# Kernel tuning notes

Hardware: AMD Instinct MI355X
Metric: run time of the kernel (lower is better)

## Reference

```python
import jax, jax.numpy as jnp
import numpy as np
from jax import lax

D_MODEL = 1024
D_STATE = 16
D_CONV = 4
D_INNER = 2 * D_MODEL
BATCH = 2
SEQ = 1024


def setup_inputs() -> dict:
    key = jax.random.key(0)
    ks = jax.random.split(key, 8)
    std = 0.02
    return {
        "x": jax.random.normal(ks[0], (BATCH, SEQ, D_MODEL), jnp.float32),
        "in_proj_w": jax.random.normal(ks[1], (2 * D_INNER, D_MODEL), jnp.float32) * std,
        "conv_w": jax.random.normal(ks[2], (D_INNER, 1, D_CONV), jnp.float32) * 0.1,
        "x_proj_w": jax.random.normal(ks[3], (D_STATE + 1, D_INNER), jnp.float32) * std,
        "dt_w": jax.random.normal(ks[4], (D_INNER, 1), jnp.float32) * std,
        "dt_b": jnp.zeros((D_INNER,), jnp.float32),
        "A_param": jax.random.normal(ks[5], (D_INNER, D_STATE), jnp.float32) * std,
        "D_param": jnp.ones((D_INNER,), jnp.float32),
        "out_w": jax.random.normal(ks[6], (D_MODEL, D_INNER), jnp.float32) * std,
        "out_b": jnp.zeros((D_MODEL,), jnp.float32),
    }


def _silu(v):
    return v * jax.nn.sigmoid(v)


def _mamba_forward(x, in_proj_w, conv_w, x_proj_w, dt_w, dt_b, A_param, D_param, out_w, out_b):
    B, L, _ = x.shape
    # in_proj: [B,L,2*d_inner]
    xz = jnp.einsum('bld,ed->ble', x, in_proj_w)
    u, z = jnp.split(xz, 2, axis=-1)  # each [B,L,d_inner]
    # depthwise causal conv1d along time
    uc = u.transpose(0, 2, 1)  # [B,d_inner,L]
    uc = lax.conv_general_dilated(
        uc, conv_w, window_strides=(1,), padding=[(D_CONV - 1, D_CONV - 1)],
        dimension_numbers=('NCH', 'OIH', 'NCH'), feature_group_count=D_INNER,
    )[:, :, :L]
    u = _silu(uc.transpose(0, 2, 1))  # [B,L,d_inner]
    # x_proj -> (dt scalar, B coeffs)
    x_dbl = jnp.einsum('bld,ed->ble', u, x_proj_w)  # [B,L,d_state+1]
    dt_in = x_dbl[..., :1]                          # [B,L,1]
    Bmat = x_dbl[..., 1:]                           # [B,L,d_state]
    delta = jax.nn.softplus(dt_in * dt_w[:, 0] + dt_b)  # [B,L,d_inner]
    A = -jnp.exp(A_param)                            # [d_inner,d_state]

    # selective scan (time-major lax.scan)
    def step(h, inp):
        d_t, b_t = inp  # [B,d_inner], [B,d_state]
        h = jnp.exp(A * d_t[..., None]) * h + d_t[..., None] * b_t[:, None, :]
        y = jnp.einsum('bdn,bn->bd', h, b_t)
        return h, y

    h0 = jnp.zeros((B, D_INNER, D_STATE), x.dtype)
    _, ys = lax.scan(step, h0, (delta.transpose(1, 0, 2), Bmat.transpose(1, 0, 2)))
    y = ys.transpose(1, 0, 2) + u * D_param  # [B,L,d_inner]
    y = y * _silu(z)
    return jnp.einsum('bld,ed->ble', y, out_w) + out_b


def reference(x, in_proj_w, conv_w, x_proj_w, dt_w, dt_b, A_param, D_param, out_w, out_b):
    return _mamba_forward(x, in_proj_w, conv_w, x_proj_w, dt_w, dt_b, A_param, D_param, out_w, out_b)
```

## Files before the change

kernel.cpp:

```cpp
#include <hip/hip_runtime.h>
#include <stdint.h>
#include <stddef.h>

#define D_MODEL 1024
#define D_STATE 16
#define D_INNER 2048
#define BATCH   2
#define SEQ     1024
#define MROWS   (BATCH*SEQ)

#define NCH 32
#define TCH (SEQ/NCH)
#define NREC (BATCH*D_INNER*D_STATE)

#define XKS 8
#define XKC (D_INNER/XKS)

typedef __bf16 bf16x8 __attribute__((ext_vector_type(8)));
typedef float  f32x4  __attribute__((ext_vector_type(4)));

__device__ __forceinline__ unsigned short f2bf(float f) {
    unsigned int u = __float_as_uint(f);
    u += 0x7fffu + ((u >> 16) & 1u);
    return (unsigned short)(u >> 16);
}
__device__ __forceinline__ float bf2f(unsigned short v) {
    return __uint_as_float((unsigned int)v << 16);
}

__device__ __forceinline__ void gl_lds16(const unsigned short* g, unsigned short* l) {
    __builtin_amdgcn_global_load_lds(
        (const __attribute__((address_space(1))) unsigned int*)g,
        (__attribute__((address_space(3))) unsigned int*)l, 16, 0, 0);
}

__global__ void cvt_all_kernel(const float* __restrict__ x,
                               const float* __restrict__ w1,
                               const float* __restrict__ w2,
                               const float* __restrict__ xw,
                               unsigned short* __restrict__ xb,
                               unsigned short* __restrict__ wbi,
                               unsigned short* __restrict__ wbo,
                               unsigned short* __restrict__ wbp) {
    int blk = blockIdx.x, tid = threadIdx.x;
    if (blk < 8192) {
        const float* src; unsigned short* dst; int i;
        if (blk < 2048)      { src = x;  dst = xb;  i = blk * 1024 + tid * 4; }
        else if (blk < 6144) { src = w1; dst = wbi; i = (blk - 2048) * 1024 + tid * 4; }
        else                 { src = w2; dst = wbo; i = (blk - 6144) * 1024 + tid * 4; }
        float4 v = *(const float4*)(src + i);
        ushort4 o;
        o.x = f2bf(v.x); o.y = f2bf(v.y); o.z = f2bf(v.z); o.w = f2bf(v.w);
        *(ushort4*)(dst + i) = o;
    } else {
        int id = (blk - 8192) * 256 + tid;
        wbp[id] = (id < 17 * D_INNER) ? f2bf(xw[id]) : (unsigned short)0;
    }
}

template<int NT, bool BIAS>
__global__ void gemm_bf16_kernel(const unsigned short* __restrict__ A,
                                 const unsigned short* __restrict__ Bw,
                                 float* __restrict__ C,
                                 const float* __restrict__ bias,
                                 int M, int N, int K) {
    constexpr int NTW  = NT / 32;
    constexpr int BCHW = NT / 64;
    __shared__ __align__(16) unsigned short Al[128 * 32];
    __shared__ __align__(16) unsigned short Bl[NT * 32];

    const int tid  = threadIdx.x;
    const int lane = tid & 63;
    const int wid  = tid >> 6;
    const int wm   = wid >> 1;
    const int wn   = wid & 1;
    const int ln   = lane & 15;
    const int q    = lane >> 4;
    const int mblk = blockIdx.y * 128;
    const int nblk = blockIdx.x * NT;
    const int srow = lane >> 2;
    const int spart = lane & 3;

    f32x4 acc[4][NTW] = {};

    for (int k0 = 0; k0 < K; k0 += 32) {
        #pragma unroll
        for (int h = 0; h < 2; ++h) {
            int j = wid * 2 + h;
            int row = j * 16 + srow;
            gl_lds16(A + (size_t)(mblk + row) * K + k0 + spart * 8, Al + j * 512);
        }
        #pragma unroll
        for (int h = 0; h < BCHW; ++h) {
            int j = wid * BCHW + h;
            int row = j * 16 + srow;
            gl_lds16(Bw + (size_t)(nblk + row) * K + k0 + spart * 8, Bl + j * 512);
        }
        __syncthreads();

        bf16x8 af[4], bfr[NTW];
        #pragma unroll
        for (int mt = 0; mt < 4; ++mt)
            af[mt] = *(const bf16x8*)(Al + (wm * 64 + mt * 16 + ln) * 32 + q * 8);
        #pragma unroll
        for (int nt = 0; nt < NTW; ++nt)
            bfr[nt] = *(const bf16x8*)(Bl + (wn * (NT/2) + nt * 16 + ln) * 32 + q * 8);

        #pragma unroll
        for (int mt = 0; mt < 4; ++mt)
            #pragma unroll
            for (int nt = 0; nt < NTW; ++nt)
                acc[mt][nt] = __builtin_amdgcn_mfma_f32_16x16x32_bf16(
                    af[mt], bfr[nt], acc[mt][nt], 0, 0, 0);
        __syncthreads();
    }

    #pragma unroll
    for (int mt = 0; mt < 4; ++mt) {
        #pragma unroll
        for (int nt = 0; nt < NTW; ++nt) {
            int col = nblk + wn * (NT/2) + nt * 16 + ln;
            float bv = BIAS ? bias[col] : 0.f;
            #pragma unroll
            for (int r = 0; r < 4; ++r) {
                int row = mblk + wm * 64 + mt * 16 + q * 4 + r;
                C[(size_t)row * N + col] = acc[mt][nt][r] + bv;
            }
        }
    }
}

__global__ void conv_silu_kernel(const float* __restrict__ xz,
                                 const float* __restrict__ conv_w,
                                 unsigned short* __restrict__ ub) {
    int idx = blockIdx.x * blockDim.x + threadIdx.x;
    int d = idx & (D_INNER - 1);
    int m = idx >> 11;
    int l = m & (SEQ - 1);
    const float* w = conv_w + d * 4;
    float s = 0.f;
    #pragma unroll
    for (int j = 0; j < 4; ++j) {
        if (l - j >= 0) s += w[3 - j] * xz[(size_t)(m - j) * 4096 + d];
    }
    float sig = 1.f / (1.f + __expf(-s));
    ub[idx] = f2bf(s * sig);
}

__global__ void xproj_mfma_kernel(const unsigned short* __restrict__ ub,
                                  const unsigned short* __restrict__ wbp,
                                  float* __restrict__ part) {
    __shared__ __align__(16) unsigned short Al[64 * 64];
    __shared__ __align__(16) unsigned short Bl[32 * 64];

    const int tid  = threadIdx.x;
    const int lane = tid & 63;
    const int wid  = tid >> 6;
    const int ln   = lane & 15;
    const int q    = lane >> 4;
    const int m0   = blockIdx.y * 64;
    const int ks   = blockIdx.x;
    const int srow = lane >> 3;
    const int spart = lane & 7;

    f32x4 acc[2] = {};

    for (int it = 0; it < 4; ++it) {
        int k0 = ks * XKC + it * 64;
        #pragma unroll
        for (int h = 0; h < 2; ++h) {
            int j = wid * 2 + h;
            int row = j * 8 + srow;
            gl_lds16(ub + (size_t)(m0 + row) * D_INNER + k0 + spart * 8, Al + j * 512);
        }
        {
            int row = wid * 8 + srow;
            gl_lds16(wbp + (size_t)row * D_INNER + k0 + spart * 8, Bl + wid * 512);
        }
        __syncthreads();

        bf16x8 af[2], bfr[2][2];
        #pragma unroll
        for (int kh = 0; kh < 2; ++kh) {
            af[kh] = *(const bf16x8*)(Al + (wid * 16 + ln) * 64 + kh * 32 + q * 8);
            bfr[0][kh] = *(const bf16x8*)(Bl + (0 * 16 + ln) * 64 + kh * 32 + q * 8);
            bfr[1][kh] = *(const bf16x8*)(Bl + (1 * 16 + ln) * 64 + kh * 32 + q * 8);
        }
        #pragma unroll
        for (int kh = 0; kh < 2; ++kh) {
            acc[0] = __builtin_amdgcn_mfma_f32_16x16x32_bf16(af[kh], bfr[0][kh], acc[0], 0, 0, 0);
            acc[1] = __builtin_amdgcn_mfma_f32_16x16x32_bf16(af[kh], bfr[1][kh], acc[1], 0, 0, 0);
        }
        __syncthreads();
    }

    #pragma unroll
    for (int nf = 0; nf < 2; ++nf) {
        #pragma unroll
        for (int r = 0; r < 4; ++r) {
            int m = m0 + wid * 16 + q * 4 + r;
            part[((size_t)ks * MROWS + m) * 32 + nf * 16 + ln] = acc[nf][r];
        }
    }
}

__global__ void xproj_reduce_kernel(const float* __restrict__ part,
                                    float* __restrict__ dti,
                                    float* __restrict__ Bm) {
    int id = blockIdx.x * 256 + threadIdx.x;
    int m = id >> 5, n = id & 31;
    float s = 0.f;
    #pragma unroll
    for (int ks = 0; ks < XKS; ++ks) s += part[(size_t)ks * MROWS * 32 + id];
    if (n == 0) dti[m] = s;
    else if (n < 17) Bm[(size_t)m * D_STATE + (n - 1)] = s;
}

__device__ __forceinline__ float softplus_f(float xv) {
    return fmaxf(xv, 0.f) + __logf(1.f + __expf(-fabsf(xv)));
}

__global__ void scanA_kernel(const float* __restrict__ dt_in,
                             const float* __restrict__ Bm,
                             const float* __restrict__ dt_w,
                             const float* __restrict__ dt_b,
                             const float* __restrict__ A_param,
                             float* __restrict__ Pg,
                             float* __restrict__ Sg) {
    __shared__ float sdt[TCH];
    __shared__ float sB[TCH * D_STATE];
    const int tid = threadIdx.x;
    const int b = blockIdx.z, c = blockIdx.y;
    const int d = blockIdx.x * 256 + tid;

    if (tid < TCH) sdt[tid] = dt_in[b * SEQ + c * TCH + tid];
    if (tid < TCH * D_STATE / 4)
        ((float4*)sB)[tid] = ((const float4*)(Bm + ((size_t)(b * SEQ + c * TCH)) * D_STATE))[tid];
    __syncthreads();

    const float dtw = dt_w[d], dtb = dt_b[d];
    float aA[D_STATE], h[D_STATE];
    #pragma unroll
    for (int n4 = 0; n4 < 4; ++n4) {
        float4 ap = ((const float4*)(A_param + (size_t)d * D_STATE))[n4];
        aA[n4*4+0] = -__expf(ap.x); aA[n4*4+1] = -__expf(ap.y);
        aA[n4*4+2] = -__expf(ap.z); aA[n4*4+3] = -__expf(ap.w);
    }
    #pragma unroll
    for (int n = 0; n < D_STATE; ++n) h[n] = 0.f;
    float tsum = 0.f;

    for (int t = 0; t < TCH; ++t) {
        float sp = softplus_f(sdt[t] * dtw + dtb);
        tsum += sp;
        #pragma unroll
        for (int n = 0; n < D_STATE; ++n) {
            float a = __expf(aA[n] * sp);
            h[n] = a * h[n] + sp * sB[t * D_STATE + n];
        }
    }

    size_t base = (size_t)c * NREC + ((size_t)(b * D_INNER + d)) * D_STATE;
    #pragma unroll
    for (int n4 = 0; n4 < 4; ++n4) {
        float4 pv, sv;
        pv.x = __expf(aA[n4*4+0] * tsum); pv.y = __expf(aA[n4*4+1] * tsum);
        pv.z = __expf(aA[n4*4+2] * tsum); pv.w = __expf(aA[n4*4+3] * tsum);
        sv.x = h[n4*4+0]; sv.y = h[n4*4+1]; sv.z = h[n4*4+2]; sv.w = h[n4*4+3];
        *(float4*)(Pg + base + n4 * 4) = pv;
        *(float4*)(Sg + base + n4 * 4) = sv;
    }
}

__global__ void scanB_kernel(const float* __restrict__ Pg,
                             const float* __restrict__ Sg,
                             float* __restrict__ Hin) {
    int idx = blockIdx.x * 256 + threadIdx.x;
    float h = 0.f;
    #pragma unroll
    for (int c = 0; c < NCH; ++c) {
        size_t o = (size_t)c * NREC + idx;
        Hin[o] = h;
        h = Pg[o] * h + Sg[o];
    }
}

__global__ void scanC_kernel(const float* __restrict__ dt_in,
                             const float* __restrict__ Bm,
                             const float* __restrict__ dt_w,
                             const float* __restrict__ dt_b,
                             const float* __restrict__ A_param,
                             const float* __restrict__ Hin,
                             const unsigned short* __restrict__ ub,
                             const float* __restrict__ xz,
                             const float* __restrict__ Dp,
                             unsigned short* __restrict__ ypb) {
    __shared__ float sdt[TCH];
    __shared__ float sB[TCH * D_STATE];
    const int tid = threadIdx.x;
    const int b = blockIdx.z, c = blockIdx.y;
    const int d = blockIdx.x * 256 + tid;

    if (tid < TCH) sdt[tid] = dt_in[b * SEQ + c * TCH + tid];
    if (tid < TCH * D_STATE / 4)
        ((float4*)sB)[tid] = ((const float4*)(Bm + ((size_t)(b * SEQ + c * TCH)) * D_STATE))[tid];
    __syncthreads();

    const float dtw = dt_w[d], dtb = dt_b[d];
    const float Dv = Dp[d];
    float aA[D_STATE], h[D_STATE];
    #pragma unroll
    for (int n4 = 0; n4 < 4; ++n4) {
        float4 ap = ((const float4*)(A_param + (size_t)d * D_STATE))[n4];
        aA[n4*4+0] = -__expf(ap.x); aA[n4*4+1] = -__expf(ap.y);
        aA[n4*4+2] = -__expf(ap.z); aA[n4*4+3] = -__expf(ap.w);
    }
    size_t hbase = (size_t)c * NREC + ((size_t)(b * D_INNER + d)) * D_STATE;
    #pragma unroll
    for (int n4 = 0; n4 < 4; ++n4) {
        float4 hv = *(const float4*)(Hin + hbase + n4 * 4);
        h[n4*4+0] = hv.x; h[n4*4+1] = hv.y; h[n4*4+2] = hv.z; h[n4*4+3] = hv.w;
    }

    const size_t mrow0 = (size_t)b * SEQ + c * TCH;
    for (int t = 0; t < TCH; ++t) {
        float sp = softplus_f(sdt[t] * dtw + dtb);
        float y0 = 0.f, y1 = 0.f, y2 = 0.f, y3 = 0.f;
        #pragma unroll
        for (int n4 = 0; n4 < 4; ++n4) {
            #pragma unroll
            for (int j = 0; j < 4; ++j) {
                int n = n4 * 4 + j;
                float Bv = sB[t * D_STATE + n];
                float a = __expf(aA[n] * sp);
                h[n] = a * h[n] + sp * Bv;
                float p = h[n] * Bv;
                if (n4 == 0) y0 += p; else if (n4 == 1) y1 += p;
                else if (n4 == 2) y2 += p; else y3 += p;
            }
        }
        float y = (y0 + y1) + (y2 + y3);
        size_t m = mrow0 + t;
        float z  = xz[m * 4096 + D_INNER + d];
        float sz = z / (1.f + __expf(-z));
        float uv = bf2f(ub[m * D_INNER + d]);
        ypb[m * D_INNER + d] = f2bf((y + uv * Dv) * sz);
    }
}

extern "C" void kernel_launch(void* const* d_in, const int* in_sizes, int n_in,
                              void* d_out, int out_size, void* d_ws, size_t ws_size,
                              hipStream_t stream) {
    const float* x         = (const float*)d_in[0];
    const float* in_proj_w = (const float*)d_in[1];
    const float* conv_w    = (const float*)d_in[2];
    const float* x_proj_w  = (const float*)d_in[3];
    const float* dt_w      = (const float*)d_in[4];
    const float* dt_b      = (const float*)d_in[5];
    const float* A_param   = (const float*)d_in[6];
    const float* D_param   = (const float*)d_in[7];
    const float* out_w     = (const float*)d_in[8];
    const float* out_b     = (const float*)d_in[9];
    float* out = (float*)d_out;

    char* ws = (char*)d_ws;
    unsigned short* xb  = (unsigned short*)(ws);
    unsigned short* wbi = (unsigned short*)(ws + (4u  << 20));
    unsigned short* wbo = (unsigned short*)(ws + (12u << 20));
    float*          xz  = (float*)(ws + (16u << 20));
    unsigned short* ub  = (unsigned short*)(ws + (48u << 20));
    float*          dti = (float*)(ws + (56u << 20));
    float*          Bm  = (float*)(ws + (56u << 20) + (64u  << 10));
    unsigned short* wbp = (unsigned short*)(ws + (56u << 20) + (192u << 10));
    float*          xpt = (float*)(ws + (56u << 20) + (512u << 10));
    float*          Pg  = (float*)(ws + (59u << 20));
    float*          Sg  = (float*)(ws + (67u << 20));
    float*          Hin = (float*)(ws + (75u << 20));
    unsigned short* ypb = (unsigned short*)(ws + (83u << 20));

    cvt_all_kernel<<<dim3(8448), 256, 0, stream>>>(
        x, in_proj_w, out_w, x_proj_w, xb, wbi, wbo, wbp);

    gemm_bf16_kernel<128, false><<<dim3(4096 / 128, MROWS / 128), 256, 0, stream>>>(
        xb, wbi, xz, nullptr, MROWS, 2 * D_INNER, D_MODEL);

    conv_silu_kernel<<<dim3(MROWS * D_INNER / 256), 256, 0, stream>>>(xz, conv_w, ub);

    xproj_mfma_kernel<<<dim3(XKS, MROWS / 64), 256, 0, stream>>>(ub, wbp, xpt);
    xproj_reduce_kernel<<<dim3(MROWS * 32 / 256), 256, 0, stream>>>(xpt, dti, Bm);

    scanA_kernel<<<dim3(D_INNER / 256, NCH, BATCH), 256, 0, stream>>>(
        dti, Bm, dt_w, dt_b, A_param, Pg, Sg);
    scanB_kernel<<<dim3(NREC / 256), 256, 0, stream>>>(Pg, Sg, Hin);
    scanC_kernel<<<dim3(D_INNER / 256, NCH, BATCH), 256, 0, stream>>>(
        dti, Bm, dt_w, dt_b, A_param, Hin, ub, xz, D_param, ypb);

    gemm_bf16_kernel<64, true><<<dim3(1024 / 64, MROWS / 128), 256, 0, stream>>>(
        ypb, wbo, out, out_b, MROWS, D_MODEL, D_INNER);
}
```

Baseline: 238.8 us.

## Store in_proj output as bf16, deepen GEMM K-step, split-K out_proj

The in_proj GEMM now writes its xz result as bf16 rather than fp32, which halves the traffic for that write and for the later reads in conv and scanC. The GEMM kernel now stages 64 K-elements per barrier pair instead of 32, so the main loop synchronises half as often. The out_proj GEMM is split into two K halves to launch more blocks, and a separate reduction kernel sums the halves and adds the bias. In exchange, xz is rounded to bf16 and the split adds an fp32 partial buffer, one extra write and read of it, and one more launch.

```diff
diff --git a/kernel.cpp b/kernel.cpp
--- a/kernel.cpp
+++ b/kernel.cpp
@@ -58,16 +58,15 @@
     }
 }
 
-template<int NT, bool BIAS>
+template<int NT, bool SPLITK2, bool OUT_BF16>
 __global__ void gemm_bf16_kernel(const unsigned short* __restrict__ A,
                                  const unsigned short* __restrict__ Bw,
-                                 float* __restrict__ C,
-                                 const float* __restrict__ bias,
+                                 void* __restrict__ Cv,
                                  int M, int N, int K) {
-    constexpr int NTW  = NT / 32;
-    constexpr int BCHW = NT / 64;
-    __shared__ __align__(16) unsigned short Al[128 * 32];
-    __shared__ __align__(16) unsigned short Bl[NT * 32];
+    constexpr int NTW = NT / 32;
+    constexpr int BCH = NT / 8;
+    __shared__ __align__(16) unsigned short Al[2 * 128 * 32];
+    __shared__ __align__(16) unsigned short Bl[2 * NT * 32];
 
     const int tid  = threadIdx.x;
     const int lane = tid & 63;
@@ -81,56 +80,82 @@
     const int srow = lane >> 2;
     const int spart = lane & 3;
 
+    const int kbeg = SPLITK2 ? blockIdx.z * (K / 2) : 0;
+    const int kend = SPLITK2 ? kbeg + K / 2 : K;
+
     f32x4 acc[4][NTW] = {};
 
-    for (int k0 = 0; k0 < K; k0 += 32) {
-        #pragma unroll
-        for (int h = 0; h < 2; ++h) {
-            int j = wid * 2 + h;
-            int row = j * 16 + srow;
-            gl_lds16(A + (size_t)(mblk + row) * K + k0 + spart * 8, Al + j * 512);
-        }
-        #pragma unroll
-        for (int h = 0; h < BCHW; ++h) {
-            int j = wid * BCHW + h;
-            int row = j * 16 + srow;
-            gl_lds16(Bw + (size_t)(nblk + row) * K + k0 + spart * 8, Bl + j * 512);
+    for (int k0 = kbeg; k0 < kend; k0 += 64) {
+        #pragma unroll
+        for (int h = 0; h < 4; ++h) {
+            int j = wid * 4 + h;
+            int kh = j & 1, rb = j >> 1;
+            int row = rb * 16 + srow;
+            gl_lds16(A + (size_t)(mblk + row) * K + k0 + kh * 32 + spart * 8,
+                     Al + kh * 4096 + rb * 512);
+        }
+        #pragma unroll
+        for (int h = 0; h < BCH / 4; ++h) {
+            int j = wid * (BCH / 4) + h;
+            int kh = j & 1, rb = j >> 1;
+            int row = rb * 16 + srow;
+            gl_lds16(Bw + (size_t)(nblk + row) * K + k0 + kh * 32 + spart * 8,
+                     Bl + kh * (NT * 32) + rb * 512);
         }
         __syncthreads();
 
-        bf16x8 af[4], bfr[NTW];
-        #pragma unroll
-        for (int mt = 0; mt < 4; ++mt)
-            af[mt] = *(const bf16x8*)(Al + (wm * 64 + mt * 16 + ln) * 32 + q * 8);
-        #pragma unroll
-        for (int nt = 0; nt < NTW; ++nt)
-            bfr[nt] = *(const bf16x8*)(Bl + (wn * (NT/2) + nt * 16 + ln) * 32 + q * 8);
-
-        #pragma unroll
-        for (int mt = 0; mt < 4; ++mt)
+        #pragma unroll
+        for (int kh = 0; kh < 2; ++kh) {
+            bf16x8 af[4], bfr[NTW];
+            #pragma unroll
+            for (int mt = 0; mt < 4; ++mt)
+                af[mt] = *(const bf16x8*)(Al + kh * 4096 + (wm * 64 + mt * 16 + ln) * 32 + q * 8);
             #pragma unroll
             for (int nt = 0; nt < NTW; ++nt)
-                acc[mt][nt] = __builtin_amdgcn_mfma_f32_16x16x32_bf16(
-                    af[mt], bfr[nt], acc[mt][nt], 0, 0, 0);
+                bfr[nt] = *(const bf16x8*)(Bl + kh * (NT * 32) + (wn * (NT/2) + nt * 16 + ln) * 32 + q * 8);
+            #pragma unroll
+            for (int mt = 0; mt < 4; ++mt)
+                #pragma unroll
+                for (int nt = 0; nt < NTW; ++nt)
+                    acc[mt][nt] = __builtin_amdgcn_mfma_f32_16x16x32_bf16(
+                        af[mt], bfr[nt], acc[mt][nt], 0, 0, 0);
+        }
         __syncthreads();
     }
 
+    size_t cofs = SPLITK2 ? (size_t)blockIdx.z * M * N : 0;
     #pragma unroll
     for (int mt = 0; mt < 4; ++mt) {
         #pragma unroll
         for (int nt = 0; nt < NTW; ++nt) {
             int col = nblk + wn * (NT/2) + nt * 16 + ln;
-            float bv = BIAS ? bias[col] : 0.f;
             #pragma unroll
             for (int r = 0; r < 4; ++r) {
                 int row = mblk + wm * 64 + mt * 16 + q * 4 + r;
-                C[(size_t)row * N + col] = acc[mt][nt][r] + bv;
+                if (OUT_BF16)
+                    ((unsigned short*)Cv)[cofs + (size_t)row * N + col] = f2bf(acc[mt][nt][r]);
+                else
+                    ((float*)Cv)[cofs + (size_t)row * N + col] = acc[mt][nt][r];
             }
         }
     }
 }
 
-__global__ void conv_silu_kernel(const float* __restrict__ xz,
+__global__ void splitk_reduce_kernel(const float* __restrict__ part,
+                                     const float* __restrict__ bias,
+                                     float* __restrict__ out) {
+    int i = (blockIdx.x * 256 + threadIdx.x) * 4;
+    int n = i & (D_MODEL - 1);
+    float4 a = *(const float4*)(part + i);
+    float4 b = *(const float4*)(part + (size_t)MROWS * D_MODEL + i);
+    float4 bv = *(const float4*)(bias + n);
+    float4 o;
+    o.x = a.x + b.x + bv.x; o.y = a.y + b.y + bv.y;
+    o.z = a.z + b.z + bv.z; o.w = a.w + b.w + bv.w;
+    *(float4*)(out + i) = o;
+}
+
+__global__ void conv_silu_kernel(const unsigned short* __restrict__ xzb,
                                  const float* __restrict__ conv_w,
                                  unsigned short* __restrict__ ub) {
     int idx = blockIdx.x * blockDim.x + threadIdx.x;
@@ -141,7 +166,7 @@
     float s = 0.f;
     #pragma unroll
     for (int j = 0; j < 4; ++j) {
-        if (l - j >= 0) s += w[3 - j] * xz[(size_t)(m - j) * 4096 + d];
+        if (l - j >= 0) s += w[3 - j] * bf2f(xzb[(size_t)(m - j) * 4096 + d]);
     }
     float sig = 1.f / (1.f + __expf(-s));
     ub[idx] = f2bf(s * sig);
@@ -292,7 +317,7 @@
                              const float* __restrict__ A_param,
                              const float* __restrict__ Hin,
                              const unsigned short* __restrict__ ub,
-                             const float* __restrict__ xz,
+                             const unsigned short* __restrict__ xzb,
                              const float* __restrict__ Dp,
                              unsigned short* __restrict__ ypb) {
     __shared__ float sdt[TCH];
@@ -341,7 +366,7 @@
         }
         float y = (y0 + y1) + (y2 + y3);
         size_t m = mrow0 + t;
-        float z  = xz[m * 4096 + D_INNER + d];
+        float z  = bf2f(xzb[m * 4096 + D_INNER + d]);
         float sz = z / (1.f + __expf(-z));
         float uv = bf2f(ub[m * D_INNER + d]);
         ypb[m * D_INNER + d] = f2bf((y + uv * Dv) * sz);
@@ -367,24 +392,25 @@
     unsigned short* xb  = (unsigned short*)(ws);
     unsigned short* wbi = (unsigned short*)(ws + (4u  << 20));
     unsigned short* wbo = (unsigned short*)(ws + (12u << 20));
-    float*          xz  = (float*)(ws + (16u << 20));
-    unsigned short* ub  = (unsigned short*)(ws + (48u << 20));
-    float*          dti = (float*)(ws + (56u << 20));
-    float*          Bm  = (float*)(ws + (56u << 20) + (64u  << 10));
-    unsigned short* wbp = (unsigned short*)(ws + (56u << 20) + (192u << 10));
-    float*          xpt = (float*)(ws + (56u << 20) + (512u << 10));
-    float*          Pg  = (float*)(ws + (59u << 20));
-    float*          Sg  = (float*)(ws + (67u << 20));
-    float*          Hin = (float*)(ws + (75u << 20));
-    unsigned short* ypb = (unsigned short*)(ws + (83u << 20));
+    unsigned short* xzb = (unsigned short*)(ws + (16u << 20));
+    unsigned short* ub  = (unsigned short*)(ws + (32u << 20));
+    float*          dti = (float*)(ws + (40u << 20));
+    float*          Bm  = (float*)(ws + (40u << 20) + (64u  << 10));
+    unsigned short* wbp = (unsigned short*)(ws + (40u << 20) + (192u << 10));
+    float*          xpt = (float*)(ws + (40u << 20) + (512u << 10));
+    float*          Pg  = (float*)(ws + (44u << 20));
+    float*          Sg  = (float*)(ws + (52u << 20));
+    float*          Hin = (float*)(ws + (60u << 20));
+    unsigned short* ypb = (unsigned short*)(ws + (68u << 20));
+    float*          g2p = (float*)(ws + (76u << 20));
 
     cvt_all_kernel<<<dim3(8448), 256, 0, stream>>>(
         x, in_proj_w, out_w, x_proj_w, xb, wbi, wbo, wbp);
 
-    gemm_bf16_kernel<128, false><<<dim3(4096 / 128, MROWS / 128), 256, 0, stream>>>(
-        xb, wbi, xz, nullptr, MROWS, 2 * D_INNER, D_MODEL);
-
-    conv_silu_kernel<<<dim3(MROWS * D_INNER / 256), 256, 0, stream>>>(xz, conv_w, ub);
+    gemm_bf16_kernel<128, false, true><<<dim3(4096 / 128, MROWS / 128), 256, 0, stream>>>(
+        xb, wbi, xzb, MROWS, 2 * D_INNER, D_MODEL);
+
+    conv_silu_kernel<<<dim3(MROWS * D_INNER / 256), 256, 0, stream>>>(xzb, conv_w, ub);
 
     xproj_mfma_kernel<<<dim3(XKS, MROWS / 64), 256, 0, stream>>>(ub, wbp, xpt);
     xproj_reduce_kernel<<<dim3(MROWS * 32 / 256), 256, 0, stream>>>(xpt, dti, Bm);
@@ -393,8 +419,10 @@
         dti, Bm, dt_w, dt_b, A_param, Pg, Sg);
     scanB_kernel<<<dim3(NREC / 256), 256, 0, stream>>>(Pg, Sg, Hin);
     scanC_kernel<<<dim3(D_INNER / 256, NCH, BATCH), 256, 0, stream>>>(
-        dti, Bm, dt_w, dt_b, A_param, Hin, ub, xz, D_param, ypb);
-
-    gemm_bf16_kernel<64, true><<<dim3(1024 / 64, MROWS / 128), 256, 0, stream>>>(
-        ypb, wbo, out, out_b, MROWS, D_MODEL, D_INNER);
-}
+        dti, Bm, dt_w, dt_b, A_param, Hin, ub, xzb, D_param, ypb);
+
+    gemm_bf16_kernel<64, true, false><<<dim3(1024 / 64, MROWS / 128, 2), 256, 0, stream>>>(
+        ypb, wbo, g2p, MROWS, D_MODEL, D_INNER);
+
+    splitk_reduce_kernel<<<dim3(MROWS * D_MODEL / 1024), 256, 0, stream>>>(g2p, out_b, out);
+}
```

Result: faster. 223.7 us (-6.3%).
